# Kernel tuning notes

Hardware: AMD Instinct MI355X
Metric: run time of the kernel (lower is better)

Reference implementation:

```python
import jax, jax.numpy as jnp
import numpy as np


def setup_inputs() -> dict:
    key = jax.random.key(0)
    k1, k2, k3, k4, k5 = jax.random.split(key, 5)
    B, A, FI = 4096, 256, 16   # batch, atoms, iso functions per atom
    Bo, FA = 512, 8            # bonds, aniso functions per bond
    return {
        "c_iso": jax.random.normal(k1, (B, A, FI), dtype=jnp.float32),
        "c_aniso": jax.random.normal(k2, (B, Bo, FA), dtype=jnp.float32),
        "int_iso": jax.random.uniform(k3, (B, A, FI), dtype=jnp.float32),
        "int_aniso": jax.random.uniform(k4, (B, Bo, FA), dtype=jnp.float32),
        "charge": jax.random.normal(k5, (B, A), dtype=jnp.float32),
    }


def reference(c_iso, c_aniso, int_iso, int_aniso, charge):
    # Bordered KKT system from the Lagrangian L(x,u) = (x-c)^T(x-c) - u (q^T x - Q):
    #   q^T x     = Q
    # Exact closed-form solution (Sherman-Morrison on the rank-1 border):
    #   u = 2 (Q - q^T c) / (q^T q),   x = c + (u/2) q
    B = c_iso.shape[0]
    c = jnp.concatenate([c_iso.reshape(B, -1), c_aniso.reshape(B, -1)], axis=1)   # [B, n]
    q = jnp.concatenate([int_iso.reshape(B, -1), int_aniso.reshape(B, -1)], axis=1)  # [B, n]
    Q = jnp.sum(charge, axis=1)                                                   # [B]
    qTc = jnp.einsum("bn,bn->b", q, c)
    qTq = jnp.einsum("bn,bn->b", q, q)
    u = 2.0 * (Q - qTc) / qTq                                                     # Lagrange multiplier [B]
    x = c + 0.5 * u[:, None] * q                                                  # [B, n]
    n_iso = c_iso.shape[1] * c_iso.shape[2]
    sol_iso = x[:, :n_iso].reshape(c_iso.shape)
    sol_aniso = x[:, n_iso:].reshape(c_aniso.shape)
    return (sol_iso, sol_aniso)
```

## Files before the change

### kernel.cpp

```cpp
#include <hip/hip_runtime.h>


#define HALF_N 4096
#define BLOCK  512

typedef float f4 __attribute__((ext_vector_type(4)));

__global__ __launch_bounds__(BLOCK, 8) void qp_charge_norm_kernel(
    const float* __restrict__ c_iso,
    const float* __restrict__ c_aniso,
    const float* __restrict__ q_iso,
    const float* __restrict__ q_aniso,
    const float* __restrict__ charge,
    float* __restrict__ out,
    int B)
{
    const int b   = blockIdx.x;
    const int tid = threadIdx.x;

    const f4* ci = (const f4*)(c_iso   + (size_t)b * HALF_N);
    const f4* ca = (const f4*)(c_aniso + (size_t)b * HALF_N);
    const f4* qi = (const f4*)(q_iso   + (size_t)b * HALF_N);
    const f4* qa = (const f4*)(q_aniso + (size_t)b * HALF_N);

    f4 cv[4], qv[4];
#pragma unroll
    for (int j = 0; j < 2; ++j) {
        cv[j]     = ci[j * BLOCK + tid];
        qv[j]     = qi[j * BLOCK + tid];
        cv[j + 2] = ca[j * BLOCK + tid];
        qv[j + 2] = qa[j * BLOCK + tid];
    }

    float qc = 0.0f, qq = 0.0f;
#pragma unroll
    for (int j = 0; j < 4; ++j) {
        qc += qv[j][0] * cv[j][0] + qv[j][1] * cv[j][1]
            + qv[j][2] * cv[j][2] + qv[j][3] * cv[j][3];
        qq += qv[j][0] * qv[j][0] + qv[j][1] * qv[j][1]
            + qv[j][2] * qv[j][2] + qv[j][3] * qv[j][3];
    }

#pragma unroll
    for (int j = 0; j < 4; ++j) {
        asm volatile("" : "+v"(cv[j]), "+v"(qv[j]));
    }

    float Qp = (tid < 256) ? charge[(size_t)b * 256 + tid] : 0.0f;

#pragma unroll
    for (int off = 32; off > 0; off >>= 1) {
        qc += __shfl_down(qc, off, 64);
        qq += __shfl_down(qq, off, 64);
        Qp += __shfl_down(Qp, off, 64);
    }

    __shared__ float s_qc[8], s_qq[8], s_Q[8];
    __shared__ float s_half_u;
    const int wave = tid >> 6;
    const int lane = tid & 63;
    if (lane == 0) { s_qc[wave] = qc; s_qq[wave] = qq; s_Q[wave] = Qp; }
    __syncthreads();
    if (tid == 0) {
        float tqc = 0.0f, tqq = 0.0f, tQ = 0.0f;
#pragma unroll
        for (int w = 0; w < 8; ++w) { tqc += s_qc[w]; tqq += s_qq[w]; tQ += s_Q[w]; }
        s_half_u = (tQ - tqc) / tqq;
    }
    __syncthreads();
    const float h = s_half_u;

    f4* oi = (f4*)(out + (size_t)b * HALF_N);
    f4* oa = (f4*)(out + (size_t)B * HALF_N + (size_t)b * HALF_N);
#pragma unroll
    for (int j = 0; j < 2; ++j) {
        f4 r = cv[j]     + h * qv[j];
        f4 s = cv[j + 2] + h * qv[j + 2];
        __builtin_nontemporal_store(r, &oi[j * BLOCK + tid]);
        __builtin_nontemporal_store(s, &oa[j * BLOCK + tid]);
    }
}

extern "C" void kernel_launch(void* const* d_in, const int* in_sizes, int n_in,
                              void* d_out, int out_size, void* d_ws, size_t ws_size,
                              hipStream_t stream) {
    const float* c_iso   = (const float*)d_in[0];
    const float* c_aniso = (const float*)d_in[1];
    const float* q_iso   = (const float*)d_in[2];
    const float* q_aniso = (const float*)d_in[3];
    const float* charge  = (const float*)d_in[4];
    float* out = (float*)d_out;

    const int B = in_sizes[0] / HALF_N;

    qp_charge_norm_kernel<<<B, BLOCK, 0, stream>>>(
        c_iso, c_aniso, q_iso, q_aniso, charge, out, B);
}
```

Measured before the change: 332.1 us.

## Assign rows to single wavefronts and recompute outputs by rereading inputs

Each wavefront now processes two batch rows on its own, reducing with wave shuffles only. This removes the shared-memory reduction and the block barriers. Instead of keeping c and q in registers, the kernel streams them in loops to compute the dot products, then reads them again to write the outputs. This relies on caches to absorb the second read and drops nontemporal stores, which risks extra memory traffic in a bandwidth-bound kernel.

```diff
diff --git a/kernel.cpp b/kernel.cpp
--- a/kernel.cpp
+++ b/kernel.cpp
@@ -2,11 +2,13 @@
 
 
 #define HALF_N 4096
-#define BLOCK  512
+#define BLOCK  256
+#define WPB    4
+#define RPW    2
 
 typedef float f4 __attribute__((ext_vector_type(4)));
 
-__global__ __launch_bounds__(BLOCK, 8) void qp_charge_norm_kernel(
+__global__ __launch_bounds__(BLOCK, 4) void qp_charge_norm_kernel(
     const float* __restrict__ c_iso,
     const float* __restrict__ c_aniso,
     const float* __restrict__ q_iso,
@@ -15,69 +17,62 @@
     float* __restrict__ out,
     int B)
 {
-    const int b   = blockIdx.x;
-    const int tid = threadIdx.x;
+    const int wave  = threadIdx.x >> 6;
+    const int lane  = threadIdx.x & 63;
+    const int gwave = blockIdx.x * WPB + wave;
 
-    const f4* ci = (const f4*)(c_iso   + (size_t)b * HALF_N);
-    const f4* ca = (const f4*)(c_aniso + (size_t)b * HALF_N);
-    const f4* qi = (const f4*)(q_iso   + (size_t)b * HALF_N);
-    const f4* qa = (const f4*)(q_aniso + (size_t)b * HALF_N);
+    for (int i = 0; i < RPW; ++i) {
+        const int b = gwave * RPW + i;
+        if (b >= B) return;
 
-    f4 cv[4], qv[4];
-#pragma unroll
-    for (int j = 0; j < 2; ++j) {
-        cv[j]     = ci[j * BLOCK + tid];
-        qv[j]     = qi[j * BLOCK + tid];
-        cv[j + 2] = ca[j * BLOCK + tid];
-        qv[j + 2] = qa[j * BLOCK + tid];
-    }
+        const f4* ci = (const f4*)(c_iso   + (size_t)b * HALF_N);
+        const f4* ca = (const f4*)(c_aniso + (size_t)b * HALF_N);
+        const f4* qi = (const f4*)(q_iso   + (size_t)b * HALF_N);
+        const f4* qa = (const f4*)(q_aniso + (size_t)b * HALF_N);
 
-    float qc = 0.0f, qq = 0.0f;
-#pragma unroll
-    for (int j = 0; j < 4; ++j) {
-        qc += qv[j][0] * cv[j][0] + qv[j][1] * cv[j][1]
-            + qv[j][2] * cv[j][2] + qv[j][3] * cv[j][3];
-        qq += qv[j][0] * qv[j][0] + qv[j][1] * qv[j][1]
-            + qv[j][2] * qv[j][2] + qv[j][3] * qv[j][3];
-    }
+        f4 ch = ((const f4*)(charge + (size_t)b * 256))[lane];
+
+        float qc0 = 0.f, qc1 = 0.f, qq0 = 0.f, qq1 = 0.f;
+#pragma unroll 8
+        for (int j = 0; j < 16; ++j) {
+            f4 c = ci[j * 64 + lane];
+            f4 q = qi[j * 64 + lane];
+            qc0 += q[0]*c[0] + q[1]*c[1] + q[2]*c[2] + q[3]*c[3];
+            qq0 += q[0]*q[0] + q[1]*q[1] + q[2]*q[2] + q[3]*q[3];
+        }
+#pragma unroll 8
+        for (int j = 0; j < 16; ++j) {
+            f4 c = ca[j * 64 + lane];
+            f4 q = qa[j * 64 + lane];
+            qc1 += q[0]*c[0] + q[1]*c[1] + q[2]*c[2] + q[3]*c[3];
+            qq1 += q[0]*q[0] + q[1]*q[1] + q[2]*q[2] + q[3]*q[3];
+        }
+        float qc = qc0 + qc1;
+        float qq = qq0 + qq1;
+        float Q  = ch[0] + ch[1] + ch[2] + ch[3];
 
 #pragma unroll
-    for (int j = 0; j < 4; ++j) {
-        asm volatile("" : "+v"(cv[j]), "+v"(qv[j]));
-    }
+        for (int off = 32; off > 0; off >>= 1) {
+            qc += __shfl_xor(qc, off, 64);
+            qq += __shfl_xor(qq, off, 64);
+            Q  += __shfl_xor(Q,  off, 64);
+        }
+        const float h = (Q - qc) / qq;
 
-    float Qp = (tid < 256) ? charge[(size_t)b * 256 + tid] : 0.0f;
-
-#pragma unroll
-    for (int off = 32; off > 0; off >>= 1) {
-        qc += __shfl_down(qc, off, 64);
-        qq += __shfl_down(qq, off, 64);
-        Qp += __shfl_down(Qp, off, 64);
-    }
-
-    __shared__ float s_qc[8], s_qq[8], s_Q[8];
-    __shared__ float s_half_u;
-    const int wave = tid >> 6;
-    const int lane = tid & 63;
-    if (lane == 0) { s_qc[wave] = qc; s_qq[wave] = qq; s_Q[wave] = Qp; }
-    __syncthreads();
-    if (tid == 0) {
-        float tqc = 0.0f, tqq = 0.0f, tQ = 0.0f;
-#pragma unroll
-        for (int w = 0; w < 8; ++w) { tqc += s_qc[w]; tqq += s_qq[w]; tQ += s_Q[w]; }
-        s_half_u = (tQ - tqc) / tqq;
-    }
-    __syncthreads();
-    const float h = s_half_u;
-
-    f4* oi = (f4*)(out + (size_t)b * HALF_N);
-    f4* oa = (f4*)(out + (size_t)B * HALF_N + (size_t)b * HALF_N);
-#pragma unroll
-    for (int j = 0; j < 2; ++j) {
-        f4 r = cv[j]     + h * qv[j];
-        f4 s = cv[j + 2] + h * qv[j + 2];
-        __builtin_nontemporal_store(r, &oi[j * BLOCK + tid]);
-        __builtin_nontemporal_store(s, &oa[j * BLOCK + tid]);
+        f4* oi = (f4*)(out + (size_t)b * HALF_N);
+        f4* oa = (f4*)(out + (size_t)B * HALF_N + (size_t)b * HALF_N);
+#pragma unroll 8
+        for (int j = 0; j < 16; ++j) {
+            f4 c = ci[j * 64 + lane];
+            f4 q = qi[j * 64 + lane];
+            oi[j * 64 + lane] = c + h * q;
+        }
+#pragma unroll 8
+        for (int j = 0; j < 16; ++j) {
+            f4 c = ca[j * 64 + lane];
+            f4 q = qa[j * 64 + lane];
+            oa[j * 64 + lane] = c + h * q;
+        }
     }
 }
 
@@ -93,6 +88,7 @@
 
     const int B = in_sizes[0] / HALF_N;
 
-    qp_charge_norm_kernel<<<B, BLOCK, 0, stream>>>(
+    const int grid = (B + WPB * RPW - 1) / (WPB * RPW);
+    qp_charge_norm_kernel<<<grid, BLOCK, 0, stream>>>(
         c_iso, c_aniso, q_iso, q_aniso, charge, out, B);
 }
```

Result: slower. 339.7 us (+2.3%).

## Process eight rows per block with double-buffered LDS prefetch of the next row

Applied to the files above, without the earlier changes.

Each block now handles eight batch rows in sequence. While the current row is computed, it prefetches the next row's q into a double-buffered LDS region with global_load_lds and the next row's c into registers. Wave roles are split: waves 0-3 handle the iso half and waves 4-7 the aniso half. Charge is read by both halves and the formula is scaled by 0.5 to compensate. The aim is to hide load latency and cut per-block launch and reduction overhead. The trade-off is fewer resident blocks (grid of B/8, launch bounds dropped to 4), manual vmcnt waits, and ordinary stores in place of nontemporal ones.

```diff
diff --git a/kernel.cpp b/kernel.cpp
--- a/kernel.cpp
+++ b/kernel.cpp
@@ -3,10 +3,24 @@
 
 #define HALF_N 4096
 #define BLOCK  512
+#define RPB    8
+#define QF4    2048
+#define WCHUNK 256
+#define SHMEM  (2 * QF4 * 16 + 2 * 32 * 4)
 
 typedef float f4 __attribute__((ext_vector_type(4)));
 
-__global__ __launch_bounds__(BLOCK, 8) void qp_charge_norm_kernel(
+__device__ __forceinline__ float dot4(f4 a, f4 b) {
+    return a[0]*b[0] + a[1]*b[1] + a[2]*b[2] + a[3]*b[3];
+}
+
+__device__ __forceinline__ void gload_lds16(const f4* gsrc, f4* lds_dst) {
+    __builtin_amdgcn_global_load_lds(
+        (const __attribute__((address_space(1))) void*)gsrc,
+        (__attribute__((address_space(3))) void*)lds_dst, 16, 0, 0);
+}
+
+__global__ __launch_bounds__(BLOCK, 4) void qp_charge_norm_kernel(
     const float* __restrict__ c_iso,
     const float* __restrict__ c_aniso,
     const float* __restrict__ q_iso,
@@ -15,69 +29,116 @@
     float* __restrict__ out,
     int B)
 {
-    const int b   = blockIdx.x;
-    const int tid = threadIdx.x;
+    extern __shared__ char smem[];
+    f4*    qbuf = (f4*)smem;
+    float* part = (float*)(smem + 2 * QF4 * 16);
 
-    const f4* ci = (const f4*)(c_iso   + (size_t)b * HALF_N);
-    const f4* ca = (const f4*)(c_aniso + (size_t)b * HALF_N);
-    const f4* qi = (const f4*)(q_iso   + (size_t)b * HALF_N);
-    const f4* qa = (const f4*)(q_aniso + (size_t)b * HALF_N);
+    const int t    = threadIdx.x;
+    const int w    = t >> 6;
+    const int lane = t & 63;
+    const bool iso = (w < 4);
+    const int  wo  = iso ? w : (w - 4);
 
-    f4 cv[4], qv[4];
+    const int b0 = blockIdx.x * RPB;
+    if (b0 >= B) return;
+    const int rows = (B - b0 < RPB) ? (B - b0) : RPB;
+
+    f4    ccur[4], cnxt[4];
+    float chg_cur, chg_nxt;
+
+    {
+        const int b = b0;
+        const f4* qsrc = iso ? (const f4*)(q_iso   + (size_t)b * HALF_N)
+                             : (const f4*)(q_aniso + (size_t)b * HALF_N);
+        const f4* csrc = iso ? (const f4*)(c_iso   + (size_t)b * HALF_N)
+                             : (const f4*)(c_aniso + (size_t)b * HALF_N);
 #pragma unroll
-    for (int j = 0; j < 2; ++j) {
-        cv[j]     = ci[j * BLOCK + tid];
-        qv[j]     = qi[j * BLOCK + tid];
-        cv[j + 2] = ca[j * BLOCK + tid];
-        qv[j + 2] = qa[j * BLOCK + tid];
+        for (int j = 0; j < 4; ++j)
+            gload_lds16(qsrc + wo * WCHUNK + j * 64 + lane,
+                        &qbuf[0 * QF4 + w * WCHUNK + j * 64]);
+#pragma unroll
+        for (int j = 0; j < 4; ++j)
+            ccur[j] = csrc[wo * WCHUNK + j * 64 + lane];
+        chg_cur = charge[(size_t)b * 256 + (t & 255)];
     }
 
-    float qc = 0.0f, qq = 0.0f;
+    for (int r = 0; r < rows; ++r) {
+        const int b = b0 + r;
+        const bool pf = (r + 1 < rows);
+
+        if (pf) {
+            const int bn = b + 1;
+            const f4* qsrc = iso ? (const f4*)(q_iso   + (size_t)bn * HALF_N)
+                                 : (const f4*)(q_aniso + (size_t)bn * HALF_N);
+            const f4* csrc = iso ? (const f4*)(c_iso   + (size_t)bn * HALF_N)
+                                 : (const f4*)(c_aniso + (size_t)bn * HALF_N);
 #pragma unroll
-    for (int j = 0; j < 4; ++j) {
-        qc += qv[j][0] * cv[j][0] + qv[j][1] * cv[j][1]
-            + qv[j][2] * cv[j][2] + qv[j][3] * cv[j][3];
-        qq += qv[j][0] * qv[j][0] + qv[j][1] * qv[j][1]
-            + qv[j][2] * qv[j][2] + qv[j][3] * qv[j][3];
-    }
+            for (int j = 0; j < 4; ++j)
+                gload_lds16(qsrc + wo * WCHUNK + j * 64 + lane,
+                            &qbuf[((r + 1) & 1) * QF4 + w * WCHUNK + j * 64]);
+#pragma unroll
+            for (int j = 0; j < 4; ++j)
+                cnxt[j] = csrc[wo * WCHUNK + j * 64 + lane];
+            chg_nxt = charge[(size_t)bn * 256 + (t & 255)];
+
+            asm volatile("s_waitcnt vmcnt(9)" ::: "memory");
+        } else if (r > 0) {
+            asm volatile("s_waitcnt vmcnt(4)" ::: "memory");
+        } else {
+            asm volatile("s_waitcnt vmcnt(0)" ::: "memory");
+        }
+        __builtin_amdgcn_sched_barrier(0);
+
+        const f4* qb = &qbuf[(r & 1) * QF4 + w * WCHUNK];
+        f4 qv[4];
+        float qc = 0.0f, qq = 0.0f;
+#pragma unroll
+        for (int j = 0; j < 4; ++j) {
+            qv[j] = qb[j * 64 + lane];
+            qc += dot4(qv[j], ccur[j]);
+            qq += dot4(qv[j], qv[j]);
+        }
+        float Qs = chg_cur;
 
 #pragma unroll
-    for (int j = 0; j < 4; ++j) {
-        asm volatile("" : "+v"(cv[j]), "+v"(qv[j]));
-    }
+        for (int off = 32; off > 0; off >>= 1) {
+            qc += __shfl_xor(qc, off, 64);
+            qq += __shfl_xor(qq, off, 64);
+            Qs += __shfl_xor(Qs, off, 64);
+        }
+        float* p = part + (r & 1) * 32;
+        if (lane == 0) {
+            p[w * 4 + 0] = qc;
+            p[w * 4 + 1] = qq;
+            p[w * 4 + 2] = Qs;
+        }
+        asm volatile("s_waitcnt lgkmcnt(0)" ::: "memory");
+        __builtin_amdgcn_s_barrier();
+        asm volatile("" ::: "memory");
+        __builtin_amdgcn_sched_barrier(0);
 
-    float Qp = (tid < 256) ? charge[(size_t)b * 256 + tid] : 0.0f;
-
-#pragma unroll
-    for (int off = 32; off > 0; off >>= 1) {
-        qc += __shfl_down(qc, off, 64);
-        qq += __shfl_down(qq, off, 64);
-        Qp += __shfl_down(Qp, off, 64);
-    }
-
-    __shared__ float s_qc[8], s_qq[8], s_Q[8];
-    __shared__ float s_half_u;
-    const int wave = tid >> 6;
-    const int lane = tid & 63;
-    if (lane == 0) { s_qc[wave] = qc; s_qq[wave] = qq; s_Q[wave] = Qp; }
-    __syncthreads();
-    if (tid == 0) {
         float tqc = 0.0f, tqq = 0.0f, tQ = 0.0f;
 #pragma unroll
-        for (int w = 0; w < 8; ++w) { tqc += s_qc[w]; tqq += s_qq[w]; tQ += s_Q[w]; }
-        s_half_u = (tQ - tqc) / tqq;
-    }
-    __syncthreads();
-    const float h = s_half_u;
+        for (int k = 0; k < 8; ++k) {
+            tqc += p[k * 4 + 0];
+            tqq += p[k * 4 + 1];
+            tQ  += p[k * 4 + 2];
+        }
+        const float h = (0.5f * tQ - tqc) / tqq;
 
-    f4* oi = (f4*)(out + (size_t)b * HALF_N);
-    f4* oa = (f4*)(out + (size_t)B * HALF_N + (size_t)b * HALF_N);
+        f4* dst = iso ? (f4*)(out + (size_t)b * HALF_N)
+                      : (f4*)(out + ((size_t)B + (size_t)b) * HALF_N);
 #pragma unroll
-    for (int j = 0; j < 2; ++j) {
-        f4 r = cv[j]     + h * qv[j];
-        f4 s = cv[j + 2] + h * qv[j + 2];
-        __builtin_nontemporal_store(r, &oi[j * BLOCK + tid]);
-        __builtin_nontemporal_store(s, &oa[j * BLOCK + tid]);
+        for (int j = 0; j < 4; ++j) {
+            f4 x = ccur[j] + h * qv[j];
+            dst[wo * WCHUNK + j * 64 + lane] = x;
+        }
+
+        if (pf) {
+#pragma unroll
+            for (int j = 0; j < 4; ++j) ccur[j] = cnxt[j];
+            chg_cur = chg_nxt;
+        }
     }
 }
 
@@ -93,6 +154,14 @@
 
     const int B = in_sizes[0] / HALF_N;
 
-    qp_charge_norm_kernel<<<B, BLOCK, 0, stream>>>(
+    static bool attr_done = false;
+    if (!attr_done) {
+        hipFuncSetAttribute((const void*)qp_charge_norm_kernel,
+                            hipFuncAttributeMaxDynamicSharedMemorySize, SHMEM);
+        attr_done = true;
+    }
+
+    const int grid = (B + RPB - 1) / RPB;
+    qp_charge_norm_kernel<<<grid, BLOCK, SHMEM, stream>>>(
         c_iso, c_aniso, q_iso, q_aniso, charge, out, B);
 }
```

Result: no change. 327.1 us (-1.5%).
